# Kernel optimization log

Measured on AMD Instinct MI355X. Metric: run time of the kernel, lower is better.

## Reference

```python
import jax, jax.numpy as jnp
import numpy as np

B, S, D, H = 4, 1024, 1024, 16
HD = D // H  # head_dim = 64
MASKED_BIAS = -10000.0


def setup_inputs() -> dict:
    key = jax.random.key(0)
    ks = jax.random.split(key, 7)
    sc = 0.02
    return {
        "hidden_states": jax.random.normal(ks[0], (B, S, D), jnp.float32),
        "textual_key": jax.random.normal(ks[1], (B, H, S, HD), jnp.float32),
        "textual_value": jax.random.normal(ks[2], (B, H, S, HD), jnp.float32),
        "Wc": jax.random.normal(ks[3], (D, 3 * D), jnp.float32) * sc,  # Conv1D c_attn
        "bc": jnp.zeros((3 * D,), jnp.float32),
        "Wp": jax.random.normal(ks[4], (D, D), jnp.float32) * sc,  # Conv1D c_proj
        "bp": jnp.zeros((D,), jnp.float32),
    }


def reference(hidden_states, textual_key, textual_value, Wc, bc, Wp, bp):
    b, s, d = hidden_states.shape
    # Conv1D: x @ W + b, then split into q, k, v
    qkv = hidden_states @ Wc + bc  # [B,S,3D]
    q, k, v = jnp.split(qkv, 3, axis=-1)

    def split_heads(t):  # [B,S,D] -> [B,H,S,HD]
        return t.reshape(b, s, H, HD).transpose(0, 2, 1, 3)

    q, k, v = split_heads(q), split_heads(k), split_heads(v)

    # cross-key scores against textual past + fused elementwise self-term
    text_w = jnp.einsum("bhqd,bhkd->bhqk", q, textual_key)  # [B,H,S,S_kv]
    self_w = jnp.sum(q * k, axis=-1, keepdims=True)  # [B,H,S,1]
    attn_w = jnp.concatenate([text_w, self_w], axis=-1) / (HD ** 0.5)

    # nonResidual causal mask: bias[kl-ql:kl, 1:kl+1] (strict lower-tri since
    # columns are shifted by 1) concatenated with an always-true self column
    i = jnp.arange(s)
    causal = i[None, :] < i[:, None]  # [S,S_kv]: allow k < q (strict)
    mask = jnp.concatenate([causal, jnp.ones((s, 1), bool)], axis=-1)[None, None]
    attn_w = jnp.where(mask, attn_w, jnp.asarray(MASKED_BIAS, attn_w.dtype))
    attn_w = jax.nn.softmax(attn_w, axis=-1)

    w_rest, w_self = attn_w[..., :-1], attn_w[..., -1:]
    out = jnp.einsum("bhqk,bhkd->bhqd", w_rest, textual_value) + w_self * v

    out = out.transpose(0, 2, 1, 3).reshape(b, s, d)  # merge heads
    return out @ Wp + bp
```

## Files before the change

### kernel.cpp

```cpp
#include <hip/hip_runtime.h>

typedef __bf16 bf16_t;
typedef __bf16 bf16x8 __attribute__((ext_vector_type(8)));
typedef __bf16 bf16x4 __attribute__((ext_vector_type(4)));
typedef _Float16 f16x4 __attribute__((ext_vector_type(4)));
typedef _Float16 f16x8 __attribute__((ext_vector_type(8)));
typedef float f32x4 __attribute__((ext_vector_type(4)));

__device__ __forceinline__ void gl_lds16(const void* g, void* l) {
  __builtin_amdgcn_global_load_lds(
      (const __attribute__((address_space(1))) unsigned int*)g,
      (__attribute__((address_space(3))) unsigned int*)l, 16, 0, 0);
}

__global__ __launch_bounds__(256) void prep_kernel(
    const float* __restrict__ hs, const float* __restrict__ tk, const float* __restrict__ tv,
    const float* __restrict__ Wc, const float* __restrict__ Wp,
    bf16_t* __restrict__ Ahs, bf16_t* __restrict__ Ktb, _Float16* __restrict__ Vtb,
    bf16_t* __restrict__ WcT, bf16_t* __restrict__ WpT) {
  const int blk = blockIdx.x;
  const int tid = threadIdx.x;
  if (blk < 4096) {
    const float4* src = (blk < 2048) ? (const float4*)hs : (const float4*)tk;
    bf16x8* dst = (blk < 2048) ? (bf16x8*)Ahs : (bf16x8*)Ktb;
    int i = (blk & 2047) * 256 + tid;
    float4 v0 = src[2 * i], v1 = src[2 * i + 1];
    bf16x8 o;
    o[0] = (bf16_t)v0.x; o[1] = (bf16_t)v0.y; o[2] = (bf16_t)v0.z; o[3] = (bf16_t)v0.w;
    o[4] = (bf16_t)v1.x; o[5] = (bf16_t)v1.y; o[6] = (bf16_t)v1.z; o[7] = (bf16_t)v1.w;
    dst[i] = o;
  } else {
    __shared__ float tile[32][65];
    const float* in; bf16_t* out; int C, r0, c0; size_t base = 0; bool isV = false;
    if (blk < 5632) {
      int t = blk - 4096; in = Wc; out = WcT; C = 3072;
      r0 = (t / 96) * 64; c0 = (t % 96) * 32;
    } else if (blk < 6144) {
      int t = blk - 5632; in = Wp; out = WpT; C = 1024;
      r0 = (t >> 5) * 64; c0 = (t & 31) * 32;
    } else {
      int t = blk - 6144; int z = t >> 5, rest = t & 31;
      in = tv; out = nullptr; isV = true; C = 64; base = (size_t)z * 65536;
      r0 = (rest >> 1) * 64; c0 = (rest & 1) * 32;
    }
    {
      int rr = tid >> 2, cq = (tid & 3) << 3;
      const float* sp = in + base + (size_t)(r0 + rr) * C + c0 + cq;
      float4 v0 = *(const float4*)sp, v1 = *(const float4*)(sp + 4);
      tile[cq + 0][rr] = v0.x; tile[cq + 1][rr] = v0.y;
      tile[cq + 2][rr] = v0.z; tile[cq + 3][rr] = v0.w;
      tile[cq + 4][rr] = v1.x; tile[cq + 5][rr] = v1.y;
      tile[cq + 6][rr] = v1.z; tile[cq + 7][rr] = v1.w;
    }
    __syncthreads();
    int y = tid >> 3, l = tid & 7;
    if (isV) {
      f16x8 o;
#pragma unroll
      for (int j = 0; j < 8; j++) {
        int k = ((l & 4) << 3) | ((j & 4) << 2) | ((l & 2) << 2) | ((l & 1) << 2) | (j & 3);
        o[j] = (_Float16)tile[y][k];
      }
      *(f16x8*)(Vtb + base + (size_t)(c0 + y) * 1024 + r0 + (l << 3)) = o;
    } else {
      const float* rowp = &tile[y][l << 3];
      bf16x8 o;
#pragma unroll
      for (int j = 0; j < 8; j++) o[j] = (bf16_t)rowp[j];
      *(bf16x8*)(out + (size_t)(c0 + y) * 1024 + r0 + (l << 3)) = o;
    }
  }
}

#define ATTN_M 12.0f
__global__ __launch_bounds__(512, 4) void fused_attn_kernel(
    const bf16_t* __restrict__ Ahs, const bf16_t* __restrict__ WcT,
    const float* __restrict__ bc,
    const bf16_t* __restrict__ Ktxt, const _Float16* __restrict__ VtxtT,
    bf16_t* __restrict__ Aout) {
  const int bh = blockIdx.x;
  const int y = blockIdx.y;
  const int qt = (y < 4) ? y : 11 - y;
  const int b = bh >> 4, h = bh & 15;
  const int tid = threadIdx.x, wave = tid >> 6, lane = tid & 63;
  const int c = lane & 15, qd = lane >> 4;
  const int i_base = qt * 128 + wave * 16;
  const int kt_max = 2 * qt + 1;
  const int m0 = b * 1024 + qt * 128;

  const bf16_t* Ktb = Ktxt + (size_t)bh * 65536;
  const _Float16* Vtb = VtxtT + (size_t)bh * 65536;

  __shared__ __align__(16) char pool[49152];
  bf16_t* Asm = (bf16_t*)pool;
  bf16_t* Bsm = (bf16_t*)(pool + 16384);
  bf16_t* Qsm = (bf16_t*)pool;
  bf16_t* KsmB = (bf16_t*)(pool + 16384);
  _Float16* VsmB = (_Float16*)(pool + 32768);

  f32x4 acc[12];
#pragma unroll
  for (int j = 0; j < 12; j++) acc[j] = (f32x4){0.f, 0.f, 0.f, 0.f};

  for (int kt = 0; kt < 16; kt++) {
#pragma unroll
    for (int p = 0; p < 2; p++) {
      int chunk = p * 512 + tid;
      int row = chunk >> 3, sb = chunk & 7, kb = sb ^ (row & 7);
      gl_lds16(Ahs + (size_t)(m0 + row) * 1024 + kt * 64 + kb * 8, Asm + chunk * 8);
    }
#pragma unroll
    for (int p = 0; p < 3; p++) {
      int chunk = p * 512 + tid;
      int brow = chunk >> 3, sb = chunk & 7, kb = sb ^ (brow & 7);
      int wrow = (brow >> 6) * 1024 + h * 64 + (brow & 63);
      gl_lds16(WcT + (size_t)wrow * 1024 + kt * 64 + kb * 8, Bsm + chunk * 8);
    }
    __syncthreads();
#pragma unroll
    for (int kk = 0; kk < 2; kk++) {
      int arow = wave * 16 + c;
      bf16x8 af = *(const bf16x8*)(&Asm[arow * 64 + (((4 * kk + qd) ^ (arow & 7)) << 3)]);
#pragma unroll
      for (int j = 0; j < 12; j++) {
        int brow = 16 * j + c;
        bf16x8 bf = *(const bf16x8*)(&Bsm[brow * 64 + (((4 * kk + qd) ^ (brow & 7)) << 3)]);
        acc[j] = __builtin_amdgcn_mfma_f32_16x16x32_bf16(af, bf, acc[j], 0, 0, 0);
      }
    }
    __syncthreads();
  }

  {
    int row = tid >> 3, sb = tid & 7, kb = sb ^ (row & 7);
    gl_lds16(Ktb + (size_t)row * 64 + kb * 8, KsmB + tid * 8);
    gl_lds16(Vtb + (size_t)row * 1024 + kb * 8, VsmB + tid * 8);
  }

#pragma unroll
  for (int j = 0; j < 12; j++) {
    float bv = bc[(j >> 2) * 1024 + h * 64 + 16 * (j & 3) + c];
#pragma unroll
    for (int r = 0; r < 4; r++) acc[j][r] += bv;
  }

  float wself[4];
#pragma unroll
  for (int r = 0; r < 4; r++) {
    float part = acc[0][r] * acc[4][r] + acc[1][r] * acc[5][r] +
                 acc[2][r] * acc[6][r] + acc[3][r] * acc[7][r];
#pragma unroll
    for (int mk = 1; mk < 16; mk <<= 1) part += __shfl_xor(part, mk, 64);
    wself[r] = __expf(part * 0.125f - ATTN_M);
  }

  f32x4 O[4];
#pragma unroll
  for (int u = 0; u < 4; u++)
#pragma unroll
    for (int r = 0; r < 4; r++) O[u][r] = wself[r] * acc[8 + u][r];

  bf16_t* Qw = Qsm + wave * 1024;
#pragma unroll
  for (int j = 0; j < 4; j++) {
#pragma unroll
    for (int r = 0; r < 4; r++) {
      int ql = 4 * qd + r, d = 16 * j + c;
      int ch = (d >> 3) ^ (ql & 7);
      Qw[ql * 64 + (ch << 3) + (d & 7)] = (bf16_t)acc[j][r];
    }
  }
  bf16x8 aq[2];
#pragma unroll
  for (int kk = 0; kk < 2; kk++) {
    int ch = (4 * kk + qd) ^ (c & 7);
    aq[kk] = *(const bf16x8*)(&Qw[c * 64 + (ch << 3)]);
  }

  float l_loc = 0.f;
  for (int kt = 0; kt <= kt_max; kt++) {
    __syncthreads();
    if (kt < kt_max) {
      int nb = (kt + 1) & 1;
      int row = tid >> 3, sb = tid & 7, kb = sb ^ (row & 7);
      gl_lds16(Ktb + (size_t)((kt + 1) * 64 + row) * 64 + kb * 8, KsmB + nb * 4096 + tid * 8);
      gl_lds16(Vtb + (size_t)row * 1024 + (kt + 1) * 64 + kb * 8, VsmB + nb * 4096 + tid * 8);
    }
    if (64 * kt >= i_base + 16) continue;
    const bf16_t* Ks = KsmB + (kt & 1) * 4096;
    const _Float16* Vs = VsmB + (kt & 1) * 4096;

    f32x4 sc[4];
#pragma unroll
    for (int t = 0; t < 4; t++) sc[t] = (f32x4){0.f, 0.f, 0.f, 0.f};
    __builtin_amdgcn_s_setprio(1);
#pragma unroll
    for (int kk = 0; kk < 2; kk++) {
#pragma unroll
      for (int t = 0; t < 4; t++) {
        int row = 16 * t + c;
        bf16x8 bk = *(const bf16x8*)(&Ks[row * 64 + (((4 * kk + qd) ^ (row & 7)) << 3)]);
        sc[t] = __builtin_amdgcn_mfma_f32_16x16x32_bf16(bk, aq[kk], sc[t], 0, 0, 0);
      }
    }
    __builtin_amdgcn_s_setprio(0);
    const bool edge = (64 * kt + 63 >= i_base);
    f16x4 pa[4];
    if (!edge) {
#pragma unroll
      for (int t = 0; t < 4; t++)
#pragma unroll
        for (int r = 0; r < 4; r++) {
          float p = __expf(sc[t][r] * 0.125f - ATTN_M);
          l_loc += p;
          pa[t][r] = (_Float16)p;
        }
    } else {
#pragma unroll
      for (int t = 0; t < 4; t++)
#pragma unroll
        for (int r = 0; r < 4; r++) {
          bool masked = (64 * kt + 16 * t + 4 * qd + r >= i_base + c);
          float p = masked ? 0.f : __expf(sc[t][r] * 0.125f - ATTN_M);
          l_loc += p;
          pa[t][r] = (_Float16)p;
        }
    }
    __builtin_amdgcn_s_setprio(1);
#pragma unroll
    for (int tp = 0; tp < 2; tp++) {
#pragma unroll
      for (int u = 0; u < 4; u++) {
        int row = 16 * u + c;
        f16x8 vv = *(const f16x8*)(&Vs[row * 64 + (((4 * tp + qd) ^ (row & 7)) << 3)]);
        f16x4 vlo = __builtin_shufflevector(vv, vv, 0, 1, 2, 3);
        f16x4 vhi = __builtin_shufflevector(vv, vv, 4, 5, 6, 7);
        O[u] = __builtin_amdgcn_mfma_f32_16x16x16f16(pa[2 * tp], vlo, O[u], 0, 0, 0);
        O[u] = __builtin_amdgcn_mfma_f32_16x16x16f16(pa[2 * tp + 1], vhi, O[u], 0, 0, 0);
      }
    }
    __builtin_amdgcn_s_setprio(0);
  }

  l_loc += __shfl_xor(l_loc, 16, 64);
  l_loc += __shfl_xor(l_loc, 32, 64);
#pragma unroll
  for (int r = 0; r < 4; r++) {
    float lq = __shfl(l_loc, 4 * qd + r, 16);
    float inv = 1.0f / (lq + wself[r]);
    int i = i_base + 4 * qd + r;
#pragma unroll
    for (int u = 0; u < 4; u++)
      Aout[((size_t)b * 1024 + i) * 1024 + h * 64 + 16 * u + c] = (bf16_t)(O[u][r] * inv);
  }
}

__global__ __launch_bounds__(256) void gemm_out_kernel(
    const bf16_t* __restrict__ A, const bf16_t* __restrict__ Bt, const float* __restrict__ bias,
    float* __restrict__ out) {
  __shared__ bf16_t Asm[2][4096];
  __shared__ bf16_t Bsm[2][8192];
  const int tid = threadIdx.x;
  const int wave = tid >> 6, lane = tid & 63;
  const int c = lane & 15, qd = lane >> 4;
  const int wn = wave * 32;
  const int m0 = blockIdx.y * 64, n0 = blockIdx.x * 128;

  f32x4 acc[4][2];
#pragma unroll
  for (int i = 0; i < 4; i++)
#pragma unroll
    for (int j = 0; j < 2; j++) acc[i][j] = (f32x4){0.f, 0.f, 0.f, 0.f};

#pragma unroll
  for (int p = 0; p < 2; p++) {
    int chunk = p * 256 + tid;
    int row = chunk >> 3, sb = chunk & 7, kb = sb ^ (row & 7);
    gl_lds16(A + (size_t)(m0 + row) * 1024 + kb * 8, &Asm[0][chunk * 8]);
  }
#pragma unroll
  for (int p = 0; p < 4; p++) {
    int chunk = p * 256 + tid;
    int row = chunk >> 3, sb = chunk & 7, kb = sb ^ (row & 7);
    gl_lds16(Bt + (size_t)(n0 + row) * 1024 + kb * 8, &Bsm[0][chunk * 8]);
  }
  for (int it = 0; it < 16; it++) {
    __syncthreads();
    if (it < 15) {
      int nbuf = (it + 1) & 1, kt = (it + 1) * 64;
#pragma unroll
      for (int p = 0; p < 2; p++) {
        int chunk = p * 256 + tid;
        int row = chunk >> 3, sb = chunk & 7, kb = sb ^ (row & 7);
        gl_lds16(A + (size_t)(m0 + row) * 1024 + kt + kb * 8, &Asm[nbuf][chunk * 8]);
      }
#pragma unroll
      for (int p = 0; p < 4; p++) {
        int chunk = p * 256 + tid;
        int row = chunk >> 3, sb = chunk & 7, kb = sb ^ (row & 7);
        gl_lds16(Bt + (size_t)(n0 + row) * 1024 + kt + kb * 8, &Bsm[nbuf][chunk * 8]);
      }
    }
    const int bs = it & 1;
#pragma unroll
    for (int kk = 0; kk < 2; kk++) {
      bf16x8 af[4], bfr[2];
#pragma unroll
      for (int i = 0; i < 4; i++) {
        int row = 16 * i + c;
        af[i] = *(const bf16x8*)(&Asm[bs][row * 64 + (((4 * kk + qd) ^ (row & 7)) << 3)]);
      }
#pragma unroll
      for (int j = 0; j < 2; j++) {
        int row = wn + 16 * j + c;
        bfr[j] = *(const bf16x8*)(&Bsm[bs][row * 64 + (((4 * kk + qd) ^ (row & 7)) << 3)]);
      }
#pragma unroll
      for (int i = 0; i < 4; i++)
#pragma unroll
        for (int j = 0; j < 2; j++)
          acc[i][j] = __builtin_amdgcn_mfma_f32_16x16x32_bf16(af[i], bfr[j], acc[i][j], 0, 0, 0);
    }
  }
#pragma unroll
  for (int j = 0; j < 2; j++) {
    int n = n0 + wn + 16 * j + c;
    float bv = bias[n];
#pragma unroll
    for (int i = 0; i < 4; i++) {
#pragma unroll
      for (int r = 0; r < 4; r++) {
        int m = m0 + 16 * i + 4 * qd + r;
        out[(size_t)m * 1024 + n] = acc[i][j][r] + bv;
      }
    }
  }
}

extern "C" void kernel_launch(void* const* d_in, const int* in_sizes, int n_in,
                              void* d_out, int out_size, void* d_ws, size_t ws_size,
                              hipStream_t stream) {
  const float* hs = (const float*)d_in[0];
  const float* tk = (const float*)d_in[1];
  const float* tv = (const float*)d_in[2];
  const float* Wc = (const float*)d_in[3];
  const float* bc = (const float*)d_in[4];
  const float* Wp = (const float*)d_in[5];
  const float* bp = (const float*)d_in[6];
  float* out = (float*)d_out;

  bf16_t* ws = (bf16_t*)d_ws;
  const size_t M1 = 1u << 20;
  bf16_t* Ahs  = ws;
  bf16_t* WcT  = ws + 4 * M1;
  bf16_t* WpT  = ws + 7 * M1;
  bf16_t* Ktb  = ws + 8 * M1;
  _Float16* Vtb = (_Float16*)(ws + 12 * M1);
  bf16_t* Aout = ws + 28 * M1;

  prep_kernel<<<8192, 256, 0, stream>>>(hs, tk, tv, Wc, Wp, Ahs, Ktb, Vtb, WcT, WpT);
  fused_attn_kernel<<<dim3(64, 8), 512, 0, stream>>>(Ahs, WcT, bc, Ktb, Vtb, Aout);
  gemm_out_kernel<<<dim3(8, 64), 256, 0, stream>>>(Aout, WpT, bp, out);
}
```

Measured before the change: 170.8 us.

## Pair complementary causal strips per block with double-buffered QKV projection

Each attention block now handles two 128-row query strips (strip s and 7-s), so every block does the same amount of causal work. Each wave owns 32 query rows, and each K/V LDS tile is reused for two MFMA row groups. The QKV projection loop is double-buffered in LDS to overlap global loads with MFMA work, which enlarges shared memory to 112KB and halves the grid to 256 blocks. This raises register and LDS pressure and lowers occupancy (launch bounds 512,2), and with fewer blocks some CUs may be left idle.

```diff
diff --git a/kernel.cpp b/kernel.cpp
--- a/kernel.cpp
+++ b/kernel.cpp
@@ -73,63 +73,77 @@
 }
 
 #define ATTN_M 12.0f
-__global__ __launch_bounds__(512, 4) void fused_attn_kernel(
+__global__ __launch_bounds__(512, 2) void fused_attn_kernel(
     const bf16_t* __restrict__ Ahs, const bf16_t* __restrict__ WcT,
     const float* __restrict__ bc,
     const bf16_t* __restrict__ Ktxt, const _Float16* __restrict__ VtxtT,
     bf16_t* __restrict__ Aout) {
   const int bh = blockIdx.x;
-  const int y = blockIdx.y;
-  const int qt = (y < 4) ? y : 11 - y;
+  const int s = blockIdx.y;
   const int b = bh >> 4, h = bh & 15;
   const int tid = threadIdx.x, wave = tid >> 6, lane = tid & 63;
   const int c = lane & 15, qd = lane >> 4;
-  const int i_base = qt * 128 + wave * 16;
-  const int kt_max = 2 * qt + 1;
-  const int m0 = b * 1024 + qt * 128;
+  const int strip = (wave < 4) ? s : 7 - s;
+  const int i_base = strip * 128 + (wave & 3) * 32;
+  const int kt_max = 15 - 2 * s;
 
   const bf16_t* Ktb = Ktxt + (size_t)bh * 65536;
   const _Float16* Vtb = VtxtT + (size_t)bh * 65536;
 
-  __shared__ __align__(16) char pool[49152];
-  bf16_t* Asm = (bf16_t*)pool;
-  bf16_t* Bsm = (bf16_t*)(pool + 16384);
-  bf16_t* Qsm = (bf16_t*)pool;
-  bf16_t* KsmB = (bf16_t*)(pool + 16384);
-  _Float16* VsmB = (_Float16*)(pool + 32768);
-
-  f32x4 acc[12];
-#pragma unroll
-  for (int j = 0; j < 12; j++) acc[j] = (f32x4){0.f, 0.f, 0.f, 0.f};
-
-  for (int kt = 0; kt < 16; kt++) {
-#pragma unroll
-    for (int p = 0; p < 2; p++) {
+  __shared__ __align__(16) char pool[114688];
+  bf16_t* AsmB = (bf16_t*)pool;
+  bf16_t* BsmB = (bf16_t*)(pool + 65536);
+  bf16_t* Qsm  = (bf16_t*)pool;
+  bf16_t* KsmB = (bf16_t*)(pool + 32768);
+  _Float16* VsmB = (_Float16*)(pool + 49152);
+
+  f32x4 acc[2][12];
+#pragma unroll
+  for (int m = 0; m < 2; m++)
+#pragma unroll
+    for (int j = 0; j < 12; j++) acc[m][j] = (f32x4){0.f, 0.f, 0.f, 0.f};
+
+  auto stage = [&](int t, int buf) {
+#pragma unroll
+    for (int p = 0; p < 4; p++) {
       int chunk = p * 512 + tid;
       int row = chunk >> 3, sb = chunk & 7, kb = sb ^ (row & 7);
-      gl_lds16(Ahs + (size_t)(m0 + row) * 1024 + kt * 64 + kb * 8, Asm + chunk * 8);
+      int grow = b * 1024 + ((row < 128) ? s * 128 + row : (7 - s) * 128 + (row - 128));
+      gl_lds16(Ahs + (size_t)grow * 1024 + t * 64 + kb * 8, AsmB + buf * 16384 + chunk * 8);
     }
 #pragma unroll
     for (int p = 0; p < 3; p++) {
       int chunk = p * 512 + tid;
       int brow = chunk >> 3, sb = chunk & 7, kb = sb ^ (brow & 7);
       int wrow = (brow >> 6) * 1024 + h * 64 + (brow & 63);
-      gl_lds16(WcT + (size_t)wrow * 1024 + kt * 64 + kb * 8, Bsm + chunk * 8);
-    }
+      gl_lds16(WcT + (size_t)wrow * 1024 + t * 64 + kb * 8, BsmB + buf * 12288 + chunk * 8);
+    }
+  };
+
+  stage(0, 0);
+  for (int kt = 0; kt < 16; kt++) {
     __syncthreads();
+    if (kt < 15) stage(kt + 1, (kt + 1) & 1);
+    const bf16_t* Acur = AsmB + (kt & 1) * 16384;
+    const bf16_t* Bcur = BsmB + (kt & 1) * 12288;
 #pragma unroll
     for (int kk = 0; kk < 2; kk++) {
-      int arow = wave * 16 + c;
-      bf16x8 af = *(const bf16x8*)(&Asm[arow * 64 + (((4 * kk + qd) ^ (arow & 7)) << 3)]);
+      bf16x8 af[2];
+#pragma unroll
+      for (int m = 0; m < 2; m++) {
+        int arow = wave * 32 + m * 16 + c;
+        af[m] = *(const bf16x8*)(&Acur[arow * 64 + (((4 * kk + qd) ^ (arow & 7)) << 3)]);
+      }
 #pragma unroll
       for (int j = 0; j < 12; j++) {
         int brow = 16 * j + c;
-        bf16x8 bf = *(const bf16x8*)(&Bsm[brow * 64 + (((4 * kk + qd) ^ (brow & 7)) << 3)]);
-        acc[j] = __builtin_amdgcn_mfma_f32_16x16x32_bf16(af, bf, acc[j], 0, 0, 0);
-      }
-    }
-    __syncthreads();
-  }
+        bf16x8 bfv = *(const bf16x8*)(&Bcur[brow * 64 + (((4 * kk + qd) ^ (brow & 7)) << 3)]);
+        acc[0][j] = __builtin_amdgcn_mfma_f32_16x16x32_bf16(af[0], bfv, acc[0][j], 0, 0, 0);
+        acc[1][j] = __builtin_amdgcn_mfma_f32_16x16x32_bf16(af[1], bfv, acc[1][j], 0, 0, 0);
+      }
+    }
+  }
+  __syncthreads();
 
   {
     int row = tid >> 3, sb = tid & 7, kb = sb ^ (row & 7);
@@ -138,46 +152,57 @@
   }
 
 #pragma unroll
-  for (int j = 0; j < 12; j++) {
-    float bv = bc[(j >> 2) * 1024 + h * 64 + 16 * (j & 3) + c];
-#pragma unroll
-    for (int r = 0; r < 4; r++) acc[j][r] += bv;
-  }
-
-  float wself[4];
-#pragma unroll
-  for (int r = 0; r < 4; r++) {
-    float part = acc[0][r] * acc[4][r] + acc[1][r] * acc[5][r] +
-                 acc[2][r] * acc[6][r] + acc[3][r] * acc[7][r];
-#pragma unroll
-    for (int mk = 1; mk < 16; mk <<= 1) part += __shfl_xor(part, mk, 64);
-    wself[r] = __expf(part * 0.125f - ATTN_M);
-  }
-
-  f32x4 O[4];
-#pragma unroll
-  for (int u = 0; u < 4; u++)
-#pragma unroll
-    for (int r = 0; r < 4; r++) O[u][r] = wself[r] * acc[8 + u][r];
-
-  bf16_t* Qw = Qsm + wave * 1024;
-#pragma unroll
-  for (int j = 0; j < 4; j++) {
+  for (int m = 0; m < 2; m++)
+#pragma unroll
+    for (int j = 0; j < 12; j++) {
+      float bv = bc[(j >> 2) * 1024 + h * 64 + 16 * (j & 3) + c];
+#pragma unroll
+      for (int r = 0; r < 4; r++) acc[m][j][r] += bv;
+    }
+
+  float wself[2][4];
+#pragma unroll
+  for (int m = 0; m < 2; m++)
 #pragma unroll
     for (int r = 0; r < 4; r++) {
-      int ql = 4 * qd + r, d = 16 * j + c;
-      int ch = (d >> 3) ^ (ql & 7);
-      Qw[ql * 64 + (ch << 3) + (d & 7)] = (bf16_t)acc[j][r];
-    }
-  }
-  bf16x8 aq[2];
-#pragma unroll
-  for (int kk = 0; kk < 2; kk++) {
-    int ch = (4 * kk + qd) ^ (c & 7);
-    aq[kk] = *(const bf16x8*)(&Qw[c * 64 + (ch << 3)]);
-  }
-
-  float l_loc = 0.f;
+      float part = acc[m][0][r] * acc[m][4][r] + acc[m][1][r] * acc[m][5][r] +
+                   acc[m][2][r] * acc[m][6][r] + acc[m][3][r] * acc[m][7][r];
+#pragma unroll
+      for (int mk = 1; mk < 16; mk <<= 1) part += __shfl_xor(part, mk, 64);
+      wself[m][r] = __expf(part * 0.125f - ATTN_M);
+    }
+
+  f32x4 O[2][4];
+#pragma unroll
+  for (int m = 0; m < 2; m++)
+#pragma unroll
+    for (int u = 0; u < 4; u++)
+#pragma unroll
+      for (int r = 0; r < 4; r++) O[m][u][r] = wself[m][r] * acc[m][8 + u][r];
+
+  bf16_t* Qw = Qsm + wave * 2048;
+#pragma unroll
+  for (int m = 0; m < 2; m++)
+#pragma unroll
+    for (int j = 0; j < 4; j++) {
+#pragma unroll
+      for (int r = 0; r < 4; r++) {
+        int ql = m * 16 + 4 * qd + r, d = 16 * j + c;
+        int ch = (d >> 3) ^ (ql & 7);
+        Qw[ql * 64 + (ch << 3) + (d & 7)] = (bf16_t)acc[m][j][r];
+      }
+    }
+  bf16x8 aq[2][2];
+#pragma unroll
+  for (int m = 0; m < 2; m++)
+#pragma unroll
+    for (int kk = 0; kk < 2; kk++) {
+      int qrow = m * 16 + c;
+      int ch = (4 * kk + qd) ^ (qrow & 7);
+      aq[m][kk] = *(const bf16x8*)(&Qw[qrow * 64 + (ch << 3)]);
+    }
+
+  float l_loc[2] = {0.f, 0.f};
   for (int kt = 0; kt <= kt_max; kt++) {
     __syncthreads();
     if (kt < kt_max) {
@@ -186,13 +211,15 @@
       gl_lds16(Ktb + (size_t)((kt + 1) * 64 + row) * 64 + kb * 8, KsmB + nb * 4096 + tid * 8);
       gl_lds16(Vtb + (size_t)row * 1024 + (kt + 1) * 64 + kb * 8, VsmB + nb * 4096 + tid * 8);
     }
-    if (64 * kt >= i_base + 16) continue;
+    if (64 * kt >= i_base + 32) continue;
     const bf16_t* Ks = KsmB + (kt & 1) * 4096;
     const _Float16* Vs = VsmB + (kt & 1) * 4096;
 
-    f32x4 sc[4];
-#pragma unroll
-    for (int t = 0; t < 4; t++) sc[t] = (f32x4){0.f, 0.f, 0.f, 0.f};
+    f32x4 sc[2][4];
+#pragma unroll
+    for (int m = 0; m < 2; m++)
+#pragma unroll
+      for (int t = 0; t < 4; t++) sc[m][t] = (f32x4){0.f, 0.f, 0.f, 0.f};
     __builtin_amdgcn_s_setprio(1);
 #pragma unroll
     for (int kk = 0; kk < 2; kk++) {
@@ -200,31 +227,34 @@
       for (int t = 0; t < 4; t++) {
         int row = 16 * t + c;
         bf16x8 bk = *(const bf16x8*)(&Ks[row * 64 + (((4 * kk + qd) ^ (row & 7)) << 3)]);
-        sc[t] = __builtin_amdgcn_mfma_f32_16x16x32_bf16(bk, aq[kk], sc[t], 0, 0, 0);
+        sc[0][t] = __builtin_amdgcn_mfma_f32_16x16x32_bf16(bk, aq[0][kk], sc[0][t], 0, 0, 0);
+        sc[1][t] = __builtin_amdgcn_mfma_f32_16x16x32_bf16(bk, aq[1][kk], sc[1][t], 0, 0, 0);
       }
     }
     __builtin_amdgcn_s_setprio(0);
-    const bool edge = (64 * kt + 63 >= i_base);
-    f16x4 pa[4];
-    if (!edge) {
-#pragma unroll
-      for (int t = 0; t < 4; t++)
-#pragma unroll
-        for (int r = 0; r < 4; r++) {
-          float p = __expf(sc[t][r] * 0.125f - ATTN_M);
-          l_loc += p;
-          pa[t][r] = (_Float16)p;
-        }
-    } else {
-#pragma unroll
-      for (int t = 0; t < 4; t++)
-#pragma unroll
-        for (int r = 0; r < 4; r++) {
-          bool masked = (64 * kt + 16 * t + 4 * qd + r >= i_base + c);
-          float p = masked ? 0.f : __expf(sc[t][r] * 0.125f - ATTN_M);
-          l_loc += p;
-          pa[t][r] = (_Float16)p;
-        }
+    f16x4 pa[2][4];
+#pragma unroll
+    for (int m = 0; m < 2; m++) {
+      if (64 * kt + 63 < i_base + 16 * m) {
+#pragma unroll
+        for (int t = 0; t < 4; t++)
+#pragma unroll
+          for (int r = 0; r < 4; r++) {
+            float p = __expf(sc[m][t][r] * 0.125f - ATTN_M);
+            l_loc[m] += p;
+            pa[m][t][r] = (_Float16)p;
+          }
+      } else {
+#pragma unroll
+        for (int t = 0; t < 4; t++)
+#pragma unroll
+          for (int r = 0; r < 4; r++) {
+            bool masked = (64 * kt + 16 * t + 4 * qd + r >= i_base + 16 * m + c);
+            float p = masked ? 0.f : __expf(sc[m][t][r] * 0.125f - ATTN_M);
+            l_loc[m] += p;
+            pa[m][t][r] = (_Float16)p;
+          }
+      }
     }
     __builtin_amdgcn_s_setprio(1);
 #pragma unroll
@@ -235,23 +265,28 @@
         f16x8 vv = *(const f16x8*)(&Vs[row * 64 + (((4 * tp + qd) ^ (row & 7)) << 3)]);
         f16x4 vlo = __builtin_shufflevector(vv, vv, 0, 1, 2, 3);
         f16x4 vhi = __builtin_shufflevector(vv, vv, 4, 5, 6, 7);
-        O[u] = __builtin_amdgcn_mfma_f32_16x16x16f16(pa[2 * tp], vlo, O[u], 0, 0, 0);
-        O[u] = __builtin_amdgcn_mfma_f32_16x16x16f16(pa[2 * tp + 1], vhi, O[u], 0, 0, 0);
+        O[0][u] = __builtin_amdgcn_mfma_f32_16x16x16f16(pa[0][2 * tp], vlo, O[0][u], 0, 0, 0);
+        O[0][u] = __builtin_amdgcn_mfma_f32_16x16x16f16(pa[0][2 * tp + 1], vhi, O[0][u], 0, 0, 0);
+        O[1][u] = __builtin_amdgcn_mfma_f32_16x16x16f16(pa[1][2 * tp], vlo, O[1][u], 0, 0, 0);
+        O[1][u] = __builtin_amdgcn_mfma_f32_16x16x16f16(pa[1][2 * tp + 1], vhi, O[1][u], 0, 0, 0);
       }
     }
     __builtin_amdgcn_s_setprio(0);
   }
 
-  l_loc += __shfl_xor(l_loc, 16, 64);
-  l_loc += __shfl_xor(l_loc, 32, 64);
-#pragma unroll
-  for (int r = 0; r < 4; r++) {
-    float lq = __shfl(l_loc, 4 * qd + r, 16);
-    float inv = 1.0f / (lq + wself[r]);
-    int i = i_base + 4 * qd + r;
-#pragma unroll
-    for (int u = 0; u < 4; u++)
-      Aout[((size_t)b * 1024 + i) * 1024 + h * 64 + 16 * u + c] = (bf16_t)(O[u][r] * inv);
+#pragma unroll
+  for (int m = 0; m < 2; m++) {
+    l_loc[m] += __shfl_xor(l_loc[m], 16, 64);
+    l_loc[m] += __shfl_xor(l_loc[m], 32, 64);
+#pragma unroll
+    for (int r = 0; r < 4; r++) {
+      float lq = __shfl(l_loc[m], 4 * qd + r, 16);
+      float inv = 1.0f / (lq + wself[m][r]);
+      int i = i_base + 16 * m + 4 * qd + r;
+#pragma unroll
+      for (int u = 0; u < 4; u++)
+        Aout[((size_t)b * 1024 + i) * 1024 + h * 64 + 16 * u + c] = (bf16_t)(O[m][u][r] * inv);
+    }
   }
 }
 
@@ -359,6 +394,6 @@
   bf16_t* Aout = ws + 28 * M1;
 
   prep_kernel<<<8192, 256, 0, stream>>>(hs, tk, tv, Wc, Wp, Ahs, Ktb, Vtb, WcT, WpT);
-  fused_attn_kernel<<<dim3(64, 8), 512, 0, stream>>>(Ahs, WcT, bc, Ktb, Vtb, Aout);
+  fused_attn_kernel<<<dim3(64, 4), 512, 0, stream>>>(Ahs, WcT, bc, Ktb, Vtb, Aout);
   gemm_out_kernel<<<dim3(8, 64), 256, 0, stream>>>(Aout, WpT, bp, out);
 }
```

Result: slower. 174.7 us (+2.3%).
